# Performance work log

Measured on AMD Instinct MI355X. Metric: run time of the kernel, lower is better.

Reference implementation:

```python
import jax, jax.numpy as jnp
import numpy as np
from jax import lax

B, C, H, W = 32, 32, 64, 64
K = 1024
DN_T = ('NCHW', 'IOHW', 'NCHW')  # conv_transpose: kernel [in, out, kh, kw]
DN_C = ('NCHW', 'OIHW', 'NCHW')  # conv:           kernel [out, in, kh, kw]


def setup_inputs() -> dict:
    key = jax.random.key(0)
    ks = jax.random.split(key, 8)
    return {
        'z': jax.random.normal(ks[0], (B, C, H, W), jnp.float32),
        'codebook': jax.random.normal(ks[1], (K, C), jnp.float32),
        'w1': jax.random.normal(ks[2], (32, 128, 4, 4), jnp.float32) * 0.05,
        'b1': jnp.zeros((128,), jnp.float32),
        'w2': jax.random.normal(ks[3], (128, 64, 4, 4), jnp.float32) * 0.05,
        'b2': jnp.zeros((64,), jnp.float32),
        'w3': jax.random.normal(ks[4], (3, 64, 3, 3), jnp.float32) * 0.05,
        'b3': jnp.zeros((3,), jnp.float32),
    }


def _quantize(z, codebook):
    # z: [B, C, H, W] -> flat [N, C]
    zf = jnp.transpose(z, (0, 2, 3, 1)).reshape(-1, z.shape[1])
    # squared distances: ||z||^2 - 2 z.E^T + ||E||^2  -> [N, K]
    d = (jnp.sum(zf * zf, axis=1, keepdims=True)
         - 2.0 * zf @ codebook.T
         + jnp.sum(codebook * codebook, axis=1))
    idx = jnp.argmin(d, axis=1)                      # [N]
    q = codebook[idx].reshape(z.shape[0], z.shape[2], z.shape[3], z.shape[1])
    q = jnp.transpose(q, (0, 3, 1, 2))               # [B, C, H, W]
    # straight-through estimator
    return z + lax.stop_gradient(q - z)


def _decode(q, w1, b1, w2, b2, w3, b3):
    x = lax.conv_transpose(q, w1, strides=(2, 2), padding='SAME',
                           dimension_numbers=DN_T) + b1[None, :, None, None]
    x = jax.nn.relu(x)                               # [B, 128, 2H, 2W]
    x = lax.conv_transpose(x, w2, strides=(2, 2), padding='SAME',
                           dimension_numbers=DN_T) + b2[None, :, None, None]
    x = jax.nn.relu(x)                               # [B, 64, 4H, 4W]
    x = lax.conv_general_dilated(x, w3, window_strides=(1, 1), padding='SAME',
                                 dimension_numbers=DN_C) + b3[None, :, None, None]
    return jax.nn.sigmoid(x)                         # [B, 3, 4H, 4W]


def reference(z, codebook, w1, b1, w2, b2, w3, b3):
    q = _quantize(z, codebook)
    return _decode(q, w1, b1, w2, b2, w3, b3)
```

## Files before the change

kernel.cpp:

```cpp
#include <hip/hip_runtime.h>
#include <hip/hip_bf16.h>


typedef __attribute__((ext_vector_type(8)))  short  bf16x8;
typedef __attribute__((ext_vector_type(4)))  float  f32x4;
typedef __attribute__((ext_vector_type(16))) float  f32x16;

static constexpr int B_=32, C_=32, H_=64, W_=64, K_=1024;
static constexpr int NPOS = B_*H_*W_;

__device__ __forceinline__ unsigned short f2bf(float f){
  unsigned u = __float_as_uint(f);
  u = u + 0x7FFFu + ((u>>16)&1u);
  return (unsigned short)(u>>16);
}
__device__ __forceinline__ float bf2f(unsigned short h){
  return __uint_as_float(((unsigned)h)<<16);
}
__device__ __forceinline__ f32x16 mfma32(bf16x8 a, bf16x8 b, f32x16 c){
  return __builtin_amdgcn_mfma_f32_32x32x16_bf16(a,b,c,0,0,0);
}
__device__ __forceinline__ f32x4 mfma16(bf16x8 a, bf16x8 b, f32x4 c){
  return __builtin_amdgcn_mfma_f32_16x16x32_bf16(a,b,c,0,0,0);
}
__device__ __forceinline__ void gload16(const void* g, void* l){
  __builtin_amdgcn_global_load_lds(
      (const __attribute__((address_space(1))) void*)(unsigned long long)g,
      (__attribute__((address_space(3))) void*)(unsigned)(unsigned long long)l,
      16, 0, 0);
}
#define WAITVM(N) asm volatile("s_waitcnt vmcnt(" #N ")" ::: "memory")
__device__ __forceinline__ void barrier_raw(){
  asm volatile("" ::: "memory");
  __builtin_amdgcn_s_barrier();
  asm volatile("" ::: "memory");
}

__global__ __launch_bounds__(256) void prep_kernel(
    const float* __restrict__ cb, const float* __restrict__ w1,
    const float* __restrict__ w2, const float* __restrict__ w3,
    double* __restrict__ cb64, double* __restrict__ e2,
    unsigned short* __restrict__ cbp_hi, unsigned short* __restrict__ cbp_lo,
    float* __restrict__ e2h,
    unsigned short* __restrict__ wt1p, unsigned short* __restrict__ wt2p,
    unsigned short* __restrict__ w3p, float* __restrict__ zpage,
    int* __restrict__ cnt) {
  int idx = blockIdx.x*256 + threadIdx.x;
  if (idx == 0) cnt[0] = 0;
  if (idx < 64) zpage[idx] = 0.f;
  if (idx < K_*C_) {
    float v = cb[idx];
    cb64[idx] = (double)v;
    unsigned short h = f2bf(v);
    cbp_hi[idx] = h;
    cbp_lo[idx] = f2bf(v - bf2f(h));
  }
  if (idx < K_) {
    double s = 0.0;
    #pragma unroll
    for (int c=0;c<C_;++c){ double v=(double)cb[idx*C_+c]; s+=v*v; }
    e2[idx] = s;
    e2h[idx] = -0.5f * (float)s;
  }
  if (idx < 65536) {
    int e=idx&7, lane=(idx>>3)&63, g=(idx>>9)&3, t=(idx>>11)&3, c=(idx>>13)&1, p=idx>>14;
    int ic = c*16 + (lane>>5)*8 + e;
    int oc = g*32 + (lane&31);
    int ky = 2*(t>>1) + (p>>1), kx = 2*(t&1) + (p&1);
    wt1p[idx] = f2bf(w1[((ic*128+oc)*4+ky)*4+kx]);
  }
  if (idx < 131072) {
    int e=idx&7, lane=(idx>>3)&63, g=(idx>>9)&1, t=(idx>>10)&3, c=(idx>>12)&3, m=(idx>>14)&1, p=idx>>15;
    int ic = m*64 + c*16 + (lane>>5)*8 + e;
    int oc = g*32 + (lane&31);
    int ky = 2*(t>>1) + (p>>1), kx = 2*(t&1) + (p&1);
    wt2p[idx] = f2bf(w2[((ic*64+oc)*4+ky)*4+kx]);
  }
  if (idx < 9216) {
    int e=idx&7, lane=(idx>>3)&63, c=(idx>>9)&1, t=idx>>10;
    int ic = c*32 + ((lane>>4)&3)*8 + e;
    int oc = lane&15;
    int dy = t/3, dx = t - 3*dy;
    w3p[idx] = (oc<3) ? f2bf(w3[((oc*64+ic)*3+dy)*3+dx]) : (unsigned short)0;
  }
}

__global__ __launch_bounds__(256) void zprep_kernel(
    const float* __restrict__ z, unsigned short* __restrict__ zth,
    unsigned short* __restrict__ ztl) {
  int n = blockIdx.x*256 + threadIdx.x;
  int b = n >> 12, hw = n & 4095;
  const float* zp = z + (((size_t)b*C_) << 12) + hw;
  unsigned short th[C_], tl[C_];
  #pragma unroll
  for (int c=0;c<C_;++c) {
    float v = zp[(size_t)c<<12];
    unsigned short h = f2bf(v);
    th[c] = h;
    tl[c] = f2bf(v - bf2f(h));
  }
  bf16x8* dh = (bf16x8*)(zth + (size_t)n*C_);
  bf16x8* dl = (bf16x8*)(ztl + (size_t)n*C_);
  #pragma unroll
  for (int v=0;v<4;++v){ dh[v]=((bf16x8*)th)[v]; dl[v]=((bf16x8*)tl)[v]; }
}

__global__ __launch_bounds__(256) void quantm_kernel(
    const unsigned short* __restrict__ zth, const unsigned short* __restrict__ ztl,
    const unsigned short* __restrict__ cbp_hi, const unsigned short* __restrict__ cbp_lo,
    const float* __restrict__ e2h, const float* __restrict__ cb,
    unsigned short* __restrict__ q, int* __restrict__ cnt, int* __restrict__ list) {
  __shared__ bf16x8 ch[1024], cl[1024];
  __shared__ float  el[256];
  int tid = threadIdx.x, lane = tid&63, wv = tid>>6;
  int m0 = blockIdx.x*128 + wv*32;
  int colL = lane&15, g = lane>>4;

  bf16x8 ah[2], al[2];
  #pragma unroll
  for (int mt=0;mt<2;++mt) {
    int pos = m0 + mt*16 + colL;
    ah[mt] = *(const bf16x8*)(zth + (size_t)pos*C_ + g*8);
    al[mt] = *(const bf16x8*)(ztl + (size_t)pos*C_ + g*8);
  }

  float b1[2][4], b2[2][4]; int i1[2][4];
  #pragma unroll
  for (int mt=0;mt<2;++mt)
    #pragma unroll
    for (int r=0;r<4;++r){ b1[mt][r]=-3e38f; b2[mt][r]=-3e38f; i1[mt][r]=0; }

  for (int cb0 = 0; cb0 < K_; cb0 += 256) {
    __syncthreads();
    {
      const bf16x8* sh = (const bf16x8*)cbp_hi + cb0*4;
      const bf16x8* sl = (const bf16x8*)cbp_lo + cb0*4;
      #pragma unroll
      for (int v=0;v<4;++v){ ch[tid + v*256] = sh[tid + v*256];
                             cl[tid + v*256] = sl[tid + v*256]; }
      el[tid] = e2h[cb0 + tid];
    }
    __syncthreads();
    #pragma unroll
    for (int nt=0; nt<16; ++nt) {
      int cloc = nt*16 + colL;
      float ei = el[cloc];
      bf16x8 bh = ch[cloc*4 + g];
      bf16x8 bl = cl[cloc*4 + g];
      int nidx = cb0 + cloc;
      #pragma unroll
      for (int mt=0;mt<2;++mt) {
        f32x4 acc = {ei, ei, ei, ei};
        acc = mfma16(al[mt], bh, acc);
        acc = mfma16(ah[mt], bl, acc);
        acc = mfma16(ah[mt], bh, acc);
        #pragma unroll
        for (int r=0;r<4;++r) {
          float s = acc[r];
          b2[mt][r] = fmaxf(b2[mt][r], fminf(s, b1[mt][r]));
          if (s > b1[mt][r]) { b1[mt][r] = s; i1[mt][r] = nidx; }
        }
      }
    }
  }

  #pragma unroll
  for (int mask=1; mask<16; mask<<=1) {
    #pragma unroll
    for (int mt=0;mt<2;++mt)
      #pragma unroll
      for (int r=0;r<4;++r) {
        float o1 = __shfl_xor(b1[mt][r], mask);
        float o2 = __shfl_xor(b2[mt][r], mask);
        int   oi = __shfl_xor(i1[mt][r], mask);
        float nb2 = fmaxf(fminf(b1[mt][r], o1), fmaxf(b2[mt][r], o2));
        if (o1 > b1[mt][r]) { b1[mt][r] = o1; i1[mt][r] = oi; }
        b2[mt][r] = nb2;
      }
  }

  #pragma unroll
  for (int mt=0;mt<2;++mt)
    #pragma unroll
    for (int r=0;r<4;++r) {
      int m = m0 + mt*16 + g*4 + r;
      int idx = i1[mt][r];
      unsigned h0 = f2bf(cb[idx*C_ + 2*colL]);
      unsigned h1 = f2bf(cb[idx*C_ + 2*colL + 1]);
      ((unsigned*)q)[(((size_t)(colL>>2))*NPOS + m)*4 + (colL&3)] = h0 | (h1<<16);
      if (colL == 0 && (b1[mt][r] - b2[mt][r]) < 0.02f) {
        int slot = atomicAdd(cnt, 1);
        list[slot] = m;
      }
    }
}

__global__ __launch_bounds__(256) void refine_kernel(
    const int* __restrict__ cnt, const int* __restrict__ list,
    const float* __restrict__ z, const double* __restrict__ cb64,
    const double* __restrict__ e2, const float* __restrict__ cb,
    unsigned short* __restrict__ q) {
  __shared__ double lcb[64*33];
  __shared__ double le2[64];
  int tid = threadIdx.x, lane = tid&63, wv = tid>>6;
  int n_ref = cnt[0];
  int stride = (int)gridDim.x * 4;
  for (int base = 0; base < n_ref; base += stride) {
    int widx = base + (int)blockIdx.x*4 + wv;
    bool active = widx < n_ref;
    int m = active ? list[widx] : 0;
    double zr[C_];
    if (active) {
      int b = m >> 12, hw = m & 4095;
      const float* zp = z + (((size_t)b*C_) << 12) + hw;
      #pragma unroll
      for (int c=0;c<C_;++c) zr[c] = (double)zp[(size_t)c<<12];
    }
    double best = -1e300; int bi = 0;
    for (int ck = 0; ck < 16; ++ck) {
      __syncthreads();
      {
        const double* src = cb64 + (size_t)ck*2048 + (size_t)tid*8;
        int row = tid >> 2, col = (tid & 3)*8;
        #pragma unroll
        for (int j=0;j<8;++j) lcb[row*33 + col + j] = src[j];
        if (tid < 64) le2[tid] = e2[ck*64 + tid];
      }
      __syncthreads();
      if (active) {
        const double* e = &lcb[lane*33];
        double a0=0,a1=0,a2=0,a3=0;
        #pragma unroll
        for (int c=0;c<C_;c+=4) {
          a0 += zr[c  ]*e[c  ]; a1 += zr[c+1]*e[c+1];
          a2 += zr[c+2]*e[c+2]; a3 += zr[c+3]*e[c+3];
        }
        double s = 2.0*((a0+a1)+(a2+a3)) - le2[lane];
        if (s > best) { best = s; bi = ck*64 + lane; }
      }
    }
    #pragma unroll
    for (int mask=1; mask<64; mask<<=1) {
      double ob = __shfl_xor(best, mask);
      int    oi = __shfl_xor(bi, mask);
      if (ob > best || (ob == best && oi < bi)) { best = ob; bi = oi; }
    }
    if (active && lane < 16) {
      unsigned h0 = f2bf(cb[bi*C_ + 2*lane]);
      unsigned h1 = f2bf(cb[bi*C_ + 2*lane + 1]);
      ((unsigned*)q)[(((size_t)(lane>>2))*NPOS + m)*4 + (lane&3)] = h0 | (h1<<16);
    }
  }
}

__global__ __launch_bounds__(256) void convt1_kernel(
    const unsigned short* __restrict__ q, const unsigned short* __restrict__ wt1p,
    const float* __restrict__ b1, const float* __restrict__ zpage,
    unsigned short* __restrict__ x1, int b0) {
  __shared__ unsigned short At[4*4*34*8];
  int tid = threadIdx.x;
  int p = tid>>6, py=(tid>>7)&1, px=(tid>>6)&1;
  int lane = tid&63, xi = lane&31, half = lane>>5, ocl = lane&31;
  int bl = blockIdx.z, b = b0 + bl;
  int Y0 = blockIdx.y*2, X0 = blockIdx.x*32;

  for (int s = tid; s < 544; s += 256) {
    int t = (s*1928)>>16;
    int c = s - t*34;
    int r = t & 3, k8 = t >> 2;
    int hg = Y0-1+r, wg = X0-1+c;
    const unsigned short* src =
        (hg>=0 && hg<64 && wg>=0 && wg<64)
            ? q + ((size_t)k8*NPOS + ((b<<12) + hg*64 + wg))*8
            : (const unsigned short*)zpage;
    *(bf16x8*)&At[s*8] = *(const bf16x8*)src;
  }
  __syncthreads();

  f32x16 acc[2][4];
  #pragma unroll
  for (int g=0;g<4;++g){
    float bv = b1[g*32+ocl];
    #pragma unroll
    for (int yr=0;yr<2;++yr){
      #pragma unroll
      for (int r=0;r<16;++r) acc[yr][g][r]=bv;
    }
  }

  #pragma unroll
  for (int c16=0;c16<2;++c16) {
    #pragma unroll
    for (int t=0;t<4;++t) {
      int j=t>>1, kx=t&1;
      int col = xi+px+kx;
      int rb = (c16*2+half)*4 + py + j;
      bf16x8 a0 = *(const bf16x8*)&At[((rb+0)*34+col)*8];
      bf16x8 a1 = *(const bf16x8*)&At[((rb+1)*34+col)*8];
      const unsigned short* wb = wt1p + ((size_t)(((p*2+c16)*4+t)*4)*64 + lane)*8;
      #pragma unroll
      for (int g=0;g<4;++g) {
        bf16x8 bf = *(const bf16x8*)(wb + g*512);
        acc[0][g] = mfma32(a0, bf, acc[0][g]);
        acc[1][g] = mfma32(a1, bf, acc[1][g]);
      }
    }
  }

  #pragma unroll
  for (int yr=0;yr<2;++yr) {
    int Y = 2*(Y0+yr)+py;
    #pragma unroll
    for (int g=0;g<4;++g) {
      int oc = g*32 + ocl, cg = oc>>3, o8 = oc&7;
      unsigned short* dst = x1 + ((((size_t)bl*16 + cg)*128 + Y)*128 + (2*X0+px))*8 + o8;
      #pragma unroll
      for (int r=0;r<16;++r) {
        int xo = (r&3) + 8*(r>>2) + 4*half;
        dst[(size_t)xo*16] = f2bf(fmaxf(acc[yr][g][r], 0.f));
      }
    }
  }
}

__global__ __launch_bounds__(512, 4) void convt2_kernel(
    const unsigned short* __restrict__ x1, const unsigned short* __restrict__ wt2p,
    const float* __restrict__ b2, const float* __restrict__ zpage,
    unsigned short* __restrict__ x2) {
  __shared__ unsigned short At[4*1024*8];
  int tid = threadIdx.x;
  int wv = __builtin_amdgcn_readfirstlane(tid>>6);
  int lane = tid&63;
  int p = wv>>1, yh = wv&1;
  int py = p>>1, px = p&1;
  int xi = lane&31, half = lane>>5, ocl = lane&31;
  int bl = blockIdx.z;
  int Y0 = blockIdx.y*4, X0 = blockIdx.x*32;

  auto issue = [&](int P) {
    int m = P>>1, h = P&1;
    const unsigned short* xsrc = x1 + ((size_t)bl*16 + m*8 + h*4)*128*128*8;
    #pragma unroll
    for (int it = 0; it < 2; ++it) {
      int u0 = it*512 + wv*64;
      int u = u0 + lane;
      int tl = (u*1928)>>16;
      int c  = u - tl*34;
      int k8 = (tl*43)>>8;
      int r  = tl - k8*6;
      int hg = Y0-1+r, wg = X0-1+c;
      bool v = (u < 816) && hg>=0 && hg<128 && wg>=0 && wg<128;
      const void* src = v ? (const void*)(xsrc + (((size_t)k8*128 + hg)*128 + wg)*8)
                          : (const void*)zpage;
      gload16(src, (void*)&At[((size_t)P*1024 + u0)*8]);
    }
  };

  f32x16 acc[2][2];
  #pragma unroll
  for (int g=0;g<2;++g){
    float bv = b2[g*32+ocl];
    #pragma unroll
    for (int yr=0;yr<2;++yr)
      #pragma unroll
      for (int r=0;r<16;++r) acc[yr][g][r]=bv;
  }

  auto compute = [&](int P) {
    int m = P>>1;
    const unsigned short* Ab = &At[(size_t)P*1024*8];
    __builtin_amdgcn_s_setprio(1);
    #pragma unroll
    for (int ci=0; ci<2; ++ci) {
      int c16 = (P&1)*2 + ci;
      #pragma unroll
      for (int t=0;t<4;++t) {
        int j=t>>1, kx=t&1;
        int col = xi+px+kx;
        int lrow = ((c16*2+half)&3)*6 + py + j + yh*2;
        bf16x8 a0 = *(const bf16x8*)&Ab[((lrow+0)*34+col)*8];
        bf16x8 a1 = *(const bf16x8*)&Ab[((lrow+1)*34+col)*8];
        const unsigned short* wb = wt2p + ((size_t)(((((p*2+m)*4+c16)*4+t)*2))*64 + lane)*8;
        bf16x8 bf0 = *(const bf16x8*)wb;
        bf16x8 bf1 = *(const bf16x8*)(wb + 512);
        acc[0][0]=mfma32(a0,bf0,acc[0][0]); acc[1][0]=mfma32(a1,bf0,acc[1][0]);
        acc[0][1]=mfma32(a0,bf1,acc[0][1]); acc[1][1]=mfma32(a1,bf1,acc[1][1]);
      }
    }
    __builtin_amdgcn_s_setprio(0);
  };

  issue(0); issue(1); issue(2);
  WAITVM(4); barrier_raw();
  compute(0);
  issue(3);
  WAITVM(4); barrier_raw();
  compute(1);
  WAITVM(2); barrier_raw();
  compute(2);
  WAITVM(0); barrier_raw();
  compute(3);

  #pragma unroll
  for (int yr=0;yr<2;++yr) {
    int Y = 2*(Y0 + yh*2 + yr) + py;
    #pragma unroll
    for (int g=0;g<2;++g) {
      int oc = g*32 + ocl, cg = oc>>3, o8 = oc&7;
      unsigned short* dst = x2 + ((((size_t)bl*8 + cg)*256 + Y)*256 + (2*X0+px))*8 + o8;
      #pragma unroll
      for (int r=0;r<16;++r) {
        int xo = (r&3) + 8*(r>>2) + 4*half;
        dst[(size_t)xo*16] = f2bf(fmaxf(acc[yr][g][r], 0.f));
      }
    }
  }
}

__global__ __launch_bounds__(512) void conv3_kernel(
    const unsigned short* __restrict__ x2, const unsigned short* __restrict__ w3p,
    const float* __restrict__ b3, const float* __restrict__ zpage,
    float* __restrict__ out, int b0) {
  __shared__ unsigned short Xt[2640*8];
  int tid = threadIdx.x, w = tid>>6, lane = tid&63;
  int xi = lane&15, k8A = (lane>>4)&3, oc = lane&15;
  int bl = blockIdx.z, b = b0 + bl;
  int y0 = blockIdx.y*8, x0 = blockIdx.x*64;
  int y = y0 + w;

  f32x4 acc[4];
  float bv = (oc<3) ? b3[oc] : 0.f;
  #pragma unroll
  for (int mt=0;mt<4;++mt){ acc[mt][0]=bv; acc[mt][1]=bv; acc[mt][2]=bv; acc[mt][3]=bv; }

  for (int c=0;c<2;++c) {
    __syncthreads();
    for (int s = tid; s < 2640; s += 512) {
      int t = (s*993)>>16;
      int cc = s - t*66;
      int k8 = (t*26)>>8;
      int r = t - k8*10;
      int rf = y0-1+r, cf = x0-1+cc;
      const unsigned short* src =
          (rf>=0 && rf<256 && cf>=0 && cf<256)
              ? x2 + ((((size_t)bl*8 + c*4 + k8)*256 + rf)*256 + cf)*8
              : (const unsigned short*)zpage;
      *(bf16x8*)&Xt[s*8] = *(const bf16x8*)src;
    }
    __syncthreads();

    #pragma unroll
    for (int t=0;t<9;++t) {
      int dy = t/3, dx = t - 3*dy;
      bf16x8 bf = *(const bf16x8*)(w3p + ((size_t)(t*2+c)*64 + lane)*8);
      #pragma unroll
      for (int mt=0;mt<4;++mt) {
        bf16x8 a = *(const bf16x8*)&Xt[((size_t)(k8A*10 + (w+dy))*66 + (mt*16 + xi + dx))*8];
        acc[mt] = mfma16(a, bf, acc[mt]);
      }
    }
  }

  if (oc < 3) {
    #pragma unroll
    for (int mt=0;mt<4;++mt) {
      f32x4 v;
      #pragma unroll
      for (int r=0;r<4;++r) v[r] = 1.f/(1.f + __expf(-acc[mt][r]));
      int x = x0 + mt*16 + ((lane>>4)&3)*4;
      *(f32x4*)(out + (((size_t)b*3 + oc)*256 + y)*256 + x) = v;
    }
  }
}

extern "C" void kernel_launch(void* const* d_in, const int* in_sizes, int n_in,
                              void* d_out, int out_size, void* d_ws, size_t ws_size,
                              hipStream_t stream) {
  const float* z  = (const float*)d_in[0];
  const float* cb = (const float*)d_in[1];
  const float* w1 = (const float*)d_in[2];
  const float* b1 = (const float*)d_in[3];
  const float* w2 = (const float*)d_in[4];
  const float* b2 = (const float*)d_in[5];
  const float* w3 = (const float*)d_in[6];
  const float* b3 = (const float*)d_in[7];
  float* out = (float*)d_out;

  char* ws = (char*)d_ws;
  size_t off = 0;
  auto alloc = [&](size_t bytes) -> void* {
    void* p = (void*)(ws + off);
    off += (bytes + 255) & ~(size_t)255;
    return p;
  };
  double* cb64         = (double*)alloc((size_t)K_*C_*8);
  double* e2           = (double*)alloc((size_t)K_*8);
  float*  zpage        = (float*)alloc(256);
  unsigned short* cbph = (unsigned short*)alloc((size_t)K_*C_*2);
  unsigned short* cbpl = (unsigned short*)alloc((size_t)K_*C_*2);
  float*  e2h          = (float*)alloc((size_t)K_*4);
  int*    cnt          = (int*)alloc(256);
  int*    list         = (int*)alloc((size_t)NPOS*4);
  unsigned short* zth  = (unsigned short*)alloc((size_t)NPOS*C_*2);
  unsigned short* ztl  = (unsigned short*)alloc((size_t)NPOS*C_*2);
  unsigned short* wt1p = (unsigned short*)alloc((size_t)65536*2);
  unsigned short* wt2p = (unsigned short*)alloc((size_t)131072*2);
  unsigned short* w3p  = (unsigned short*)alloc((size_t)9216*2);
  unsigned short* q    = (unsigned short*)alloc((size_t)NPOS*C_*2);
  size_t fixed = off;

  size_t per_b = ((size_t)16*128*128*8 + (size_t)8*256*256*8) * 2;
  long long avail = (long long)ws_size - (long long)fixed;
  int chunk = (avail >= (long long)per_b) ? (int)(avail / (long long)per_b) : 1;
  if (chunk > B_) chunk = B_;
  if      (chunk >= 32) chunk = 32;
  else if (chunk >= 16) chunk = 16;
  else if (chunk >=  8) chunk =  8;
  else if (chunk >=  4) chunk =  4;
  else if (chunk >=  2) chunk =  2;
  else                  chunk =  1;
  unsigned short* x1 = (unsigned short*)alloc((size_t)chunk*16*128*128*8*2);
  unsigned short* x2 = (unsigned short*)alloc((size_t)chunk*8*256*256*8*2);

  prep_kernel<<<512, 256, 0, stream>>>(cb, w1, w2, w3, cb64, e2, cbph, cbpl,
                                       e2h, wt1p, wt2p, w3p, zpage, cnt);
  zprep_kernel<<<512, 256, 0, stream>>>(z, zth, ztl);
  quantm_kernel<<<1024, 256, 0, stream>>>(zth, ztl, cbph, cbpl, e2h, cb,
                                          q, cnt, list);
  refine_kernel<<<512, 256, 0, stream>>>(cnt, list, z, cb64, e2, cb, q);

  for (int b0 = 0; b0 < B_; b0 += chunk) {
    int nb = (B_ - b0 < chunk) ? (B_ - b0) : chunk;
    convt1_kernel<<<dim3(2,32,nb), 256, 0, stream>>>(q, wt1p, b1, zpage, x1, b0);
    convt2_kernel<<<dim3(4,32,nb), 512, 0, stream>>>(x1, wt2p, b2, zpage, x2);
    conv3_kernel <<<dim3(4,32,nb), 512, 0, stream>>>(x2, w3p, b3, zpage, out, b0);
  }
}
```

Measured before the change: 437.0 us.

## Double-buffer conv3 input tiles with async global-to-LDS loads and narrower tiles

The conv3 kernel now loads its two channel halves into separate LDS buffers using direct global-to-LDS loads (gload16), so the second half streams in while the first half is being computed. The tile width is halved from 64 to 32 columns and the grid doubled, giving more blocks and less LDS per block per stage. The cost is more halo overhead relative to tile size (34 vs 66 columns), and fewer MFMAs per wave to hide the remaining latency.

```diff
diff --git a/kernel.cpp b/kernel.cpp
--- a/kernel.cpp
+++ b/kernel.cpp
@@ -421,49 +421,59 @@
     const unsigned short* __restrict__ x2, const unsigned short* __restrict__ w3p,
     const float* __restrict__ b3, const float* __restrict__ zpage,
     float* __restrict__ out, int b0) {
-  __shared__ unsigned short Xt[2640*8];
+  __shared__ unsigned short Xt[2][1536*8];
   int tid = threadIdx.x, w = tid>>6, lane = tid&63;
   int xi = lane&15, k8A = (lane>>4)&3, oc = lane&15;
   int bl = blockIdx.z, b = b0 + bl;
-  int y0 = blockIdx.y*8, x0 = blockIdx.x*64;
+  int y0 = blockIdx.y*8, x0 = blockIdx.x*32;
   int y = y0 + w;
 
-  f32x4 acc[4];
-  float bv = (oc<3) ? b3[oc] : 0.f;
-  #pragma unroll
-  for (int mt=0;mt<4;++mt){ acc[mt][0]=bv; acc[mt][1]=bv; acc[mt][2]=bv; acc[mt][3]=bv; }
-
-  for (int c=0;c<2;++c) {
-    __syncthreads();
-    for (int s = tid; s < 2640; s += 512) {
-      int t = (s*993)>>16;
-      int cc = s - t*66;
+  auto stage = [&](int c, int buf) {
+    #pragma unroll
+    for (int i=0;i<3;++i) {
+      int sbase = i*512 + w*64;
+      int s = sbase + lane;
+      int t = (s*1928)>>16;
+      int cc = s - t*34;
       int k8 = (t*26)>>8;
       int r = t - k8*10;
       int rf = y0-1+r, cf = x0-1+cc;
-      const unsigned short* src =
-          (rf>=0 && rf<256 && cf>=0 && cf<256)
-              ? x2 + ((((size_t)bl*8 + c*4 + k8)*256 + rf)*256 + cf)*8
-              : (const unsigned short*)zpage;
-      *(bf16x8*)&Xt[s*8] = *(const bf16x8*)src;
-    }
-    __syncthreads();
-
+      bool ok = (s < 1360) && rf>=0 && rf<256 && cf>=0 && cf<256;
+      const void* src = ok
+          ? (const void*)(x2 + ((((size_t)bl*8 + c*4 + k8)*256 + rf)*256 + cf)*8)
+          : (const void*)zpage;
+      gload16(src, (void*)&Xt[buf][sbase*8]);
+    }
+  };
+
+  f32x4 acc[2];
+  float bv = (oc<3) ? b3[oc] : 0.f;
+  acc[0][0]=bv; acc[0][1]=bv; acc[0][2]=bv; acc[0][3]=bv;
+  acc[1][0]=bv; acc[1][1]=bv; acc[1][2]=bv; acc[1][3]=bv;
+
+  auto compute = [&](int c, int buf) {
     #pragma unroll
     for (int t=0;t<9;++t) {
       int dy = t/3, dx = t - 3*dy;
       bf16x8 bf = *(const bf16x8*)(w3p + ((size_t)(t*2+c)*64 + lane)*8);
       #pragma unroll
-      for (int mt=0;mt<4;++mt) {
-        bf16x8 a = *(const bf16x8*)&Xt[((size_t)(k8A*10 + (w+dy))*66 + (mt*16 + xi + dx))*8];
+      for (int mt=0;mt<2;++mt) {
+        bf16x8 a = *(const bf16x8*)&Xt[buf][((size_t)(k8A*10 + (w+dy))*34 + (mt*16 + xi + dx))*8];
         acc[mt] = mfma16(a, bf, acc[mt]);
       }
     }
-  }
+  };
+
+  stage(0, 0);
+  WAITVM(0); barrier_raw();
+  stage(1, 1);
+  compute(0, 0);
+  WAITVM(0); barrier_raw();
+  compute(1, 1);
 
   if (oc < 3) {
     #pragma unroll
-    for (int mt=0;mt<4;++mt) {
+    for (int mt=0;mt<2;++mt) {
       f32x4 v;
       #pragma unroll
       for (int r=0;r<4;++r) v[r] = 1.f/(1.f + __expf(-acc[mt][r]));
@@ -533,6 +543,6 @@
     int nb = (B_ - b0 < chunk) ? (B_ - b0) : chunk;
     convt1_kernel<<<dim3(2,32,nb), 256, 0, stream>>>(q, wt1p, b1, zpage, x1, b0);
     convt2_kernel<<<dim3(4,32,nb), 512, 0, stream>>>(x1, wt2p, b2, zpage, x2);
-    conv3_kernel <<<dim3(4,32,nb), 512, 0, stream>>>(x2, w3p, b3, zpage, out, b0);
-  }
-}
+    conv3_kernel <<<dim3(8,32,nb), 512, 0, stream>>>(x2, w3p, b3, zpage, out, b0);
+  }
+}
```

New measurement: 440.0 us. Within noise of the previous version (+0.7%).
